# Optimization experiments

Measured on AMD Instinct MI355X. Metric: run time of the kernel, lower is better.

The kernel has to match this reference:

```python
import jax, jax.numpy as jnp
import numpy as np

EPS_NORM = 1e-12  # F.normalize eps
EPS_LOG = 1e-10
COMMITMENT_COST = 0.25


def setup_inputs() -> dict:
    key = jax.random.key(0)
    k1, k2 = jax.random.split(key)
    x = jax.random.normal(k1, (32, 256, 32, 32), dtype=jnp.float32)
    # nn.Embedding weight init: uniform(-1, 1)
    W = jax.random.uniform(k2, (1024, 256), dtype=jnp.float32, minval=-1.0, maxval=1.0)
    return {"x": x, "W": W, "n": 2}


def reference(x, W, n):
    sg = jax.lax.stop_gradient
    # NCHW -> NHWC
    inputs = jnp.transpose(x, (0, 2, 3, 1))
    B, H, Wd, D = inputs.shape
    K = W.shape[0]
    flat = inputs.reshape(-1, D)                       # [N, D]
    N = flat.shape[0]
    # squared euclidean distances via matmul: [N, K]
    distances = (jnp.sum(flat * flat, axis=1, keepdims=True)
                 + jnp.sum(W * W, axis=1)
                 - 2.0 * jnp.matmul(flat, W.T))
    # topk of -distances -> n smallest distances
    neg_vals, encoding_indices = jax.lax.top_k(-distances, n)  # [N, n]
    inv_dist = 1.0 / (-neg_vals)                        # 1/distance, [N, n]
    norm = jnp.maximum(jnp.sqrt(jnp.sum(inv_dist * inv_dist, axis=-1, keepdims=True)), EPS_NORM)
    weights = sg(inv_dist / norm)                       # detached in torch
    # scatter weights into one-hot-ish encodings [N, K]
    rows = jnp.arange(N)[:, None]
    encodings = jnp.zeros((N, K), dtype=flat.dtype).at[rows, encoding_indices].set(weights)
    quantized = jnp.matmul(encodings, W).reshape(B, H, Wd, D)
    e_latent_loss = jnp.mean((sg(quantized) - inputs) ** 2)
    q_latent_loss = jnp.mean((quantized - sg(inputs)) ** 2)
    loss = q_latent_loss + COMMITMENT_COST * e_latent_loss
    # straight-through
    quantized_st = inputs + sg(quantized - inputs)
    avg_probs = jnp.mean(encodings, axis=0)
    perplexity = jnp.exp(-jnp.sum(avg_probs * jnp.log(avg_probs + EPS_LOG)))
    return loss, jnp.transpose(quantized_st, (0, 3, 1, 2)), perplexity, encodings
```

## Files before the change

kernel.cpp:

```cpp
#include <hip/hip_runtime.h>
#include <math.h>

#define NROWS 32768
#define DIMS  256
#define KCODES 1024

typedef __attribute__((ext_vector_type(8))) short short8;
typedef __attribute__((ext_vector_type(4))) float f32x4;

static const size_t OFF_WB     = 8388608;
static const size_t OFF_WNORM  = OFF_WB + 131072;
static const size_t OFF_ENCSUM = OFF_WNORM + 1024;
static const size_t OFF_LOSSP  = OFF_ENCSUM + 1024;
static const size_t OFF_WND    = OFF_LOSSP + 8192;

static const size_t OUT_Q    = 1;
static const size_t OUT_PERP = 8388609;
static const size_t OUT_ENC  = 8388610;

__device__ inline unsigned short f2bf(float f) {
    unsigned int u = __float_as_uint(f);
    unsigned int r = u + 0x7FFFu + ((u >> 16) & 1u);
    return (unsigned short)(r >> 16);
}

__device__ inline float packdi(float d, int code) {
    return __uint_as_float((__float_as_uint(d) & 0xFFFFFC00u) | (unsigned)code);
}

__device__ __forceinline__ void gl_lds16(const void* gsrc, void* ldst) {
    typedef const __attribute__((address_space(1))) unsigned int GU;
    typedef __attribute__((address_space(3))) unsigned int LU;
    __builtin_amdgcn_global_load_lds((GU*)gsrc, (LU*)ldst, 16, 0, 0);
}

__global__ __launch_bounds__(256) void wprep(const float* __restrict__ Wm,
                                             unsigned short* __restrict__ Wb,
                                             float* __restrict__ wnorm,
                                             double* __restrict__ wnormd,
                                             float* __restrict__ enc_sum)
{
    const int r = blockIdx.x * 4 + (threadIdx.x >> 6);
    const int lane = threadIdx.x & 63;
    float4 v = ((const float4*)(Wm + (size_t)r * 256))[lane];
    ushort4 o;
    o.x = f2bf(v.x); o.y = f2bf(v.y); o.z = f2bf(v.z); o.w = f2bf(v.w);
    const int d0 = lane * 4;
    const int kk = d0 >> 5, quad = (d0 >> 3) & 3, jb = d0 & 7;
    const int tt = r >> 4, col = r & 15;
    const size_t idx = (size_t)tt * 4096 + (size_t)((kk * 4 + quad) * 16 + col) * 8 + jb;
    *(ushort4*)(Wb + idx) = o;
    double s = (double)v.x*(double)v.x + (double)v.y*(double)v.y
             + (double)v.z*(double)v.z + (double)v.w*(double)v.w;
    #pragma unroll
    for (int off = 32; off > 0; off >>= 1) s += __shfl_down(s, off);
    if (lane == 0) { wnormd[r] = s; wnorm[r] = (float)s; }
    if (blockIdx.x == 0) {
        #pragma unroll
        for (int q = 0; q < 4; ++q) enc_sum[threadIdx.x * 4 + q] = 0.0f;
    }
}

__global__ __launch_bounds__(512, 4) void gemm_topk_quant(
    const float* __restrict__ x, const unsigned short* __restrict__ Wb,
    const float* __restrict__ wnorm, const double* __restrict__ wnd,
    const float* __restrict__ Wm,
    float* __restrict__ enc_sum,
    float* __restrict__ enc,
    float* __restrict__ outq, float* __restrict__ loss_part)
{
    __shared__ __align__(16) char lds[65536];
    float*  sCd   = (float*)lds;
    float*  qtile = (float*)lds;
    double* rd    = (double*)(lds + 34816);
    double* rnr   = (double*)(lds + 38912);
    int*    s0    = (int*)(lds + 39424);
    int*    s1    = (int*)(lds + 39680);
    float*  sw0   = (float*)(lds + 39936);
    float*  sw1   = (float*)(lds + 40192);
    double* sredd = (double*)(lds + 40448);
    int*    mIdx  = (int*)(lds + 40960);
    unsigned short* xtile = (unsigned short*)(lds + 32768);

    const int t    = threadIdx.x;
    const int wave = t >> 6;
    const int g    = wave & 3;
    const int h    = wave >> 2;
    const int lane = t & 63;
    const int col  = lane & 15;
    const int quad = lane >> 4;
    const int r0   = blockIdx.x * 64;
    const int b    = r0 >> 10;
    const int hw0  = r0 & 1023;
    const float* xblk = x + (size_t)b * 262144 + hw0;

    const int row = t >> 3;
    const int q8  = t & 7;

    const char* wb_bytes = (const char*)Wb;
    const size_t src_wave = (size_t)h * 262144 + (size_t)g * 4096;
    const int    lds_wave = h * 16384 + g * 4096;
    {
        const char* src = wb_bytes + src_wave;
        char* dstl = lds + lds_wave;
        #pragma unroll
        for (int q = 0; q < 4; ++q)
            gl_lds16(src + q * 1024 + lane * 16, dstl + q * 1024);
    }

    float xs[32];
    {
        const float* xr = xblk + row;
        #pragma unroll
        for (int p2 = 0; p2 < 2; ++p2)
            #pragma unroll
            for (int j = 0; j < 16; ++j)
                xs[p2 * 16 + j] = xr[(size_t)(p2 * 128 + q8 * 16 + j) * 1024];
    }

    #pragma unroll
    for (int p2 = 0; p2 < 2; ++p2)
        #pragma unroll
        for (int j4 = 0; j4 < 4; ++j4) {
            ushort4 o;
            o.x = f2bf(xs[p2 * 16 + j4 * 4 + 0]);
            o.y = f2bf(xs[p2 * 16 + j4 * 4 + 1]);
            o.z = f2bf(xs[p2 * 16 + j4 * 4 + 2]);
            o.w = f2bf(xs[p2 * 16 + j4 * 4 + 3]);
            *(ushort4*)(xtile + row * 256 + p2 * 128 + q8 * 16 + j4 * 4) = o;
        }
    __syncthreads();

    short8 af[8];
    #pragma unroll
    for (int kk = 0; kk < 8; ++kk)
        af[kk] = *(const short8*)(xtile + (g * 16 + col) * 256 + kk * 32 + quad * 8);
    __syncthreads();

    float m0[4], m1[4], m2[4];
    #pragma unroll
    for (int r = 0; r < 4; ++r) { m0[r] = 3.4e38f; m1[r] = 3.4e38f; m2[r] = 3.4e38f; }

    for (int cc = 0; cc < 16; ++cc) {
        if (cc < 15) {
            const char* src = wb_bytes + src_wave + (size_t)(cc + 1) * 16384;
            char* dstl = lds + ((cc + 1) & 1) * 32768 + lds_wave;
            #pragma unroll
            for (int q = 0; q < 4; ++q)
                gl_lds16(src + q * 1024 + lane * 16, dstl + q * 1024);
        }
        const char* bb = lds + (cc & 1) * 32768 + h * 16384;
        f32x4 acc0 = {0.f, 0.f, 0.f, 0.f};
        f32x4 acc1 = {0.f, 0.f, 0.f, 0.f};
        #pragma unroll
        for (int kk = 0; kk < 8; ++kk) {
            short8 b0 = *(const short8*)(bb + kk * 1024 + lane * 16);
            short8 b1 = *(const short8*)(bb + 8192 + kk * 1024 + lane * 16);
            acc0 = __builtin_amdgcn_mfma_f32_16x16x32_bf16(af[kk], b0, acc0, 0, 0, 0);
            acc1 = __builtin_amdgcn_mfma_f32_16x16x32_bf16(af[kk], b1, acc1, 0, 0, 0);
        }
        const int code0 = h * 512 + cc * 32 + col;
        const int code1 = code0 + 16;
        const float wn0 = wnorm[code0];
        const float wn1 = wnorm[code1];
        #pragma unroll
        for (int r = 0; r < 4; ++r) {
            float pv0 = packdi(fmaf(-2.0f, acc0[r], wn0), code0);
            float t0  = fmaxf(m0[r], pv0); m0[r] = fminf(m0[r], pv0);
            float t1  = fmaxf(m1[r], t0);  m1[r] = fminf(m1[r], t0);
            m2[r] = fminf(m2[r], t1);
            float pv1 = packdi(fmaf(-2.0f, acc1[r], wn1), code1);
            t0 = fmaxf(m0[r], pv1); m0[r] = fminf(m0[r], pv1);
            t1 = fmaxf(m1[r], t0);  m1[r] = fminf(m1[r], t0);
            m2[r] = fminf(m2[r], t1);
        }
        __syncthreads();
    }

    #pragma unroll
    for (int r = 0; r < 4; ++r) {
        int rl = g * 16 + quad * 4 + r;
        sCd[rl * 96 + h * 48 + col * 3 + 0] = m0[r];
        sCd[rl * 96 + h * 48 + col * 3 + 1] = m1[r];
        sCd[rl * 96 + h * 48 + col * 3 + 2] = m2[r];
    }
    __syncthreads();

    if (t < 64) {
        float bd[8];
        #pragma unroll
        for (int q = 0; q < 8; ++q) bd[q] = 3.4e38f;
        for (int s = 0; s < 96; ++s) {
            float d = sCd[t * 96 + s];
            if (d < bd[7]) {
                bd[7] = d;
                #pragma unroll
                for (int p = 7; p > 0; --p) {
                    if (bd[p] < bd[p-1]) { float tf = bd[p]; bd[p] = bd[p-1]; bd[p-1] = tf; }
                }
            }
        }
        #pragma unroll
        for (int q = 0; q < 8; ++q)
            mIdx[t * 8 + q] = (int)(__float_as_uint(bd[q]) & 1023u);
    }
    __syncthreads();

    {
        int cd[8];
        #pragma unroll
        for (int c8 = 0; c8 < 8; ++c8) cd[c8] = mIdx[row * 8 + c8];
        double dot[8];
        #pragma unroll
        for (int c8 = 0; c8 < 8; ++c8) dot[c8] = 0.0;
        double rn = 0.0;
        #pragma unroll
        for (int v = 0; v < 8; ++v) {
            const int d0 = (v >> 2) * 128 + q8 * 16 + (v & 3) * 4;
            const double x0 = (double)xs[v * 4 + 0];
            const double x1 = (double)xs[v * 4 + 1];
            const double x2 = (double)xs[v * 4 + 2];
            const double x3 = (double)xs[v * 4 + 3];
            rn += x0*x0 + x1*x1 + x2*x2 + x3*x3;
            #pragma unroll
            for (int c8 = 0; c8 < 8; ++c8) {
                const float4 wv = *(const float4*)(Wm + (size_t)cd[c8] * 256 + d0);
                dot[c8] += x0 * (double)wv.x + x1 * (double)wv.y
                         + x2 * (double)wv.z + x3 * (double)wv.w;
            }
        }
        #pragma unroll
        for (int m = 1; m < 8; m <<= 1) {
            #pragma unroll
            for (int c8 = 0; c8 < 8; ++c8) dot[c8] += __shfl_xor(dot[c8], m);
            rn += __shfl_xor(rn, m);
        }
        int myc = 0; double mydot = 0.0;
        #pragma unroll
        for (int c8 = 0; c8 < 8; ++c8)
            if (q8 == c8) { myc = cd[c8]; mydot = dot[c8]; }
        rd[row * 8 + q8] = wnd[myc] - 2.0 * mydot;
        if (q8 == 0) rnr[row] = rn;
    }
    __syncthreads();

    if (t < 64) {
        double rn = rnr[t];
        double d0 = 1e300, d1 = 1e300; int b0 = 1 << 30, b1 = 1 << 30;
        #pragma unroll
        for (int q = 0; q < 8; ++q) {
            double d = rd[t * 8 + q];
            int    c = mIdx[t * 8 + q];
            if (d < d0 || (d == d0 && c < b0)) { d1 = d0; b1 = b0; d0 = d; b0 = c; }
            else if (d < d1 || (d == d1 && c < b1)) { d1 = d; b1 = c; }
        }
        double D0 = rn + d0;
        double D1 = rn + d1;
        double inv0 = 1.0 / D0, inv1 = 1.0 / D1;
        double nrm = sqrt(inv0 * inv0 + inv1 * inv1);
        if (nrm < 1e-12) nrm = 1e-12;
        float w0 = (float)(inv0 / nrm);
        float w1 = (float)(inv1 / nrm);
        s0[t] = b0; s1[t] = b1; sw0[t] = w0; sw1[t] = w1;
        atomicAdd(&enc_sum[b0], w0);
        atomicAdd(&enc_sum[b1], w1);
    }
    __syncthreads();

    #pragma unroll
    for (int rr = 0; rr < 8; ++rr) {
        const int rw = wave * 8 + rr;
        const int i0 = s0[rw], i1 = s1[rw];
        const float w0 = sw0[rw], w1 = sw1[rw];
        f32x4* dst = (f32x4*)(enc + (size_t)(r0 + rw) * KCODES);
        #pragma unroll
        for (int it = 0; it < 4; ++it) {
            const int base = it * 256 + lane * 4;
            f32x4 v;
            v.x = (base + 0 == i0) ? w0 : ((base + 0 == i1) ? w1 : 0.0f);
            v.y = (base + 1 == i0) ? w0 : ((base + 1 == i1) ? w1 : 0.0f);
            v.z = (base + 2 == i0) ? w0 : ((base + 2 == i1) ? w1 : 0.0f);
            v.w = (base + 3 == i0) ? w0 : ((base + 3 == i1) ? w1 : 0.0f);
            __builtin_nontemporal_store(v, &dst[it * 64 + lane]);
        }
    }

    double ls = 0.0;
    #pragma unroll
    for (int p2 = 0; p2 < 2; ++p2) {
        const int   cA = s0[row], cB = s1[row];
        const float w0 = sw0[row], w1 = sw1[row];
        const float* W0 = Wm + (size_t)cA * 256 + p2 * 128 + q8 * 16;
        const float* W1 = Wm + (size_t)cB * 256 + p2 * 128 + q8 * 16;
        #pragma unroll
        for (int v4 = 0; v4 < 4; ++v4) {
            const float4 a  = *(const float4*)(W0 + v4 * 4);
            const float4 bv = *(const float4*)(W1 + v4 * 4);
            float q0 = w0 * a.x + w1 * bv.x;
            float q1 = w0 * a.y + w1 * bv.y;
            float q2 = w0 * a.z + w1 * bv.z;
            float q3 = w0 * a.w + w1 * bv.w;
            float e0 = q0 - xs[p2 * 16 + v4 * 4 + 0];
            float e1 = q1 - xs[p2 * 16 + v4 * 4 + 1];
            float e2 = q2 - xs[p2 * 16 + v4 * 4 + 2];
            float e3 = q3 - xs[p2 * 16 + v4 * 4 + 3];
            ls += (double)(e0*e0 + e1*e1 + e2*e2 + e3*e3);
            const int dl = q8 * 16 + v4 * 4;
            qtile[(dl + 0) * 67 + row] = q0;
            qtile[(dl + 1) * 67 + row] = q1;
            qtile[(dl + 2) * 67 + row] = q2;
            qtile[(dl + 3) * 67 + row] = q3;
        }
        __syncthreads();
        #pragma unroll
        for (int p = 0; p < 4; ++p) {
            const int task = p * 512 + t;
            const int cl   = task >> 4;
            const int hwq  = task & 15;
            f32x4 v;
            v.x = qtile[cl * 67 + hwq * 4 + 0];
            v.y = qtile[cl * 67 + hwq * 4 + 1];
            v.z = qtile[cl * 67 + hwq * 4 + 2];
            v.w = qtile[cl * 67 + hwq * 4 + 3];
            __builtin_nontemporal_store(v,
                (f32x4*)(outq + ((size_t)(b * 256 + p2 * 128 + cl)) * 1024 + hw0 + hwq * 4));
        }
        __syncthreads();
    }

    #pragma unroll
    for (int off = 32; off > 0; off >>= 1) ls += __shfl_down(ls, off);
    if (lane == 0) sredd[wave] = ls;
    __syncthreads();
    if (t == 0) {
        double s = 0.0;
        #pragma unroll
        for (int w = 0; w < 8; ++w) s += sredd[w];
        loss_part[blockIdx.x] = (float)s;
    }
}

__global__ __launch_bounds__(256) void finalize_k(const float* __restrict__ enc_sum,
                                                  const float* __restrict__ loss_part,
                                                  float* __restrict__ out)
{
    __shared__ double sh[256];
    const int t = threadIdx.x;
    double ls = 0.0;
    for (int i = t; i < 512; i += 256) ls += (double)loss_part[i];
    sh[t] = ls; __syncthreads();
    for (int s = 128; s > 0; s >>= 1) { if (t < s) sh[t] += sh[t + s]; __syncthreads(); }
    double loss_sum = sh[0];
    __syncthreads();
    double ps = 0.0;
    for (int k = t; k < KCODES; k += 256) {
        double p = (double)enc_sum[k] / (double)NROWS;
        ps += p * log(p + 1e-10);
    }
    sh[t] = ps; __syncthreads();
    for (int s = 128; s > 0; s >>= 1) { if (t < s) sh[t] += sh[t + s]; __syncthreads(); }
    if (t == 0) {
        out[0]        = (float)(1.25 * loss_sum / 8388608.0);
        out[OUT_PERP] = (float)exp(-sh[0]);
    }
}

extern "C" void kernel_launch(void* const* d_in, const int* in_sizes, int n_in,
                              void* d_out, int out_size, void* d_ws, size_t ws_size,
                              hipStream_t stream)
{
    const float* x  = (const float*)d_in[0];
    const float* Wm = (const float*)d_in[1];
    float* out = (float*)d_out;
    float* ws  = (float*)d_ws;

    unsigned short* Wb      = (unsigned short*)(ws + OFF_WB);
    float*          wnorm   = ws + OFF_WNORM;
    float*          enc_sum = ws + OFF_ENCSUM;
    float*          loss_p  = ws + OFF_LOSSP;
    double*         wnd     = (double*)(ws + OFF_WND);

    wprep<<<KCODES / 4, 256, 0, stream>>>(Wm, Wb, wnorm, wnd, enc_sum);
    gemm_topk_quant<<<NROWS / 64, 512, 0, stream>>>(x, Wb, wnorm, wnd, Wm, enc_sum,
                                                    out + OUT_ENC, out + OUT_Q, loss_p);
    finalize_k<<<1, 256, 0, stream>>>(enc_sum, loss_p, out);
}
```

Before: 272.3 us.

## Swizzle x tile in LDS, parallelize candidate merge across lanes, drop nontemporal stores

The bf16 x tile in LDS is now XOR-swizzled by row so the MFMA fragment reads hit fewer bank conflicts. The top-8 candidate merge, which used to run serially in 64 threads over 96 candidates, is now split across all threads: each of 8 lanes per row keeps a local top-8 of 12 candidates, then the lanes merge with xor shuffles. The candidate buffer is transposed to match. The encodings and quantized outputs now use ordinary stores instead of nontemporal stores, which changes how they interact with the cache.

```diff
diff --git a/kernel.cpp b/kernel.cpp
--- a/kernel.cpp
+++ b/kernel.cpp
@@ -127,14 +127,17 @@
             o.y = f2bf(xs[p2 * 16 + j4 * 4 + 1]);
             o.z = f2bf(xs[p2 * 16 + j4 * 4 + 2]);
             o.w = f2bf(xs[p2 * 16 + j4 * 4 + 3]);
-            *(ushort4*)(xtile + row * 256 + p2 * 128 + q8 * 16 + j4 * 4) = o;
+            const int xi = (row * 256 + p2 * 128 + q8 * 16 + j4 * 4) ^ ((row & 7) << 3);
+            *(ushort4*)(xtile + xi) = o;
         }
     __syncthreads();
 
     short8 af[8];
     #pragma unroll
-    for (int kk = 0; kk < 8; ++kk)
-        af[kk] = *(const short8*)(xtile + (g * 16 + col) * 256 + kk * 32 + quad * 8);
+    for (int kk = 0; kk < 8; ++kk) {
+        const int xi = ((g * 16 + col) * 256 + kk * 32 + quad * 8) ^ ((col & 7) << 3);
+        af[kk] = *(const short8*)(xtile + xi);
+    }
     __syncthreads();
 
     float m0[4], m1[4], m2[4];
@@ -179,30 +182,43 @@
 
     #pragma unroll
     for (int r = 0; r < 4; ++r) {
-        int rl = g * 16 + quad * 4 + r;
-        sCd[rl * 96 + h * 48 + col * 3 + 0] = m0[r];
-        sCd[rl * 96 + h * 48 + col * 3 + 1] = m1[r];
-        sCd[rl * 96 + h * 48 + col * 3 + 2] = m2[r];
-    }
-    __syncthreads();
-
-    if (t < 64) {
-        float bd[8];
-        #pragma unroll
-        for (int q = 0; q < 8; ++q) bd[q] = 3.4e38f;
-        for (int s = 0; s < 96; ++s) {
-            float d = sCd[t * 96 + s];
-            if (d < bd[7]) {
-                bd[7] = d;
-                #pragma unroll
-                for (int p = 7; p > 0; --p) {
-                    if (bd[p] < bd[p-1]) { float tf = bd[p]; bd[p] = bd[p-1]; bd[p-1] = tf; }
-                }
+        const int rl = g * 16 + quad * 4 + r;
+        const int s  = h * 48 + col * 3;
+        sCd[(s + 0) * 66 + rl] = m0[r];
+        sCd[(s + 1) * 66 + rl] = m1[r];
+        sCd[(s + 2) * 66 + rl] = m2[r];
+    }
+    __syncthreads();
+
+    {
+        float a0 = 3.4e38f, a1 = 3.4e38f, a2 = 3.4e38f, a3 = 3.4e38f,
+              a4 = 3.4e38f, a5 = 3.4e38f, a6 = 3.4e38f, a7 = 3.4e38f;
+        #pragma unroll
+        for (int i = 0; i < 12; ++i) {
+            float d = sCd[(q8 * 12 + i) * 66 + row];
+            if (d < a7) {
+                a7 = d; float tf;
+                if (a7 < a6) { tf = a7; a7 = a6; a6 = tf; }
+                if (a6 < a5) { tf = a6; a6 = a5; a5 = tf; }
+                if (a5 < a4) { tf = a5; a5 = a4; a4 = tf; }
+                if (a4 < a3) { tf = a4; a4 = a3; a3 = tf; }
+                if (a3 < a2) { tf = a3; a3 = a2; a2 = tf; }
+                if (a2 < a1) { tf = a2; a2 = a1; a1 = tf; }
+                if (a1 < a0) { tf = a1; a1 = a0; a0 = tf; }
             }
         }
-        #pragma unroll
-        for (int q = 0; q < 8; ++q)
-            mIdx[t * 8 + q] = (int)(__float_as_uint(bd[q]) & 1023u);
+        float sel = 3.4e38f;
+        #pragma unroll
+        for (int q = 0; q < 8; ++q) {
+            float m = a0;
+            m = fminf(m, __shfl_xor(m, 1));
+            m = fminf(m, __shfl_xor(m, 2));
+            m = fminf(m, __shfl_xor(m, 4));
+            if (q8 == q) sel = m;
+            if (a0 == m) { a0 = a1; a1 = a2; a2 = a3; a3 = a4;
+                           a4 = a5; a5 = a6; a6 = a7; a7 = 3.4e38f; }
+        }
+        mIdx[row * 8 + q8] = (int)(__float_as_uint(sel) & 1023u);
     }
     __syncthreads();
 
@@ -281,7 +297,7 @@
             v.y = (base + 1 == i0) ? w0 : ((base + 1 == i1) ? w1 : 0.0f);
             v.z = (base + 2 == i0) ? w0 : ((base + 2 == i1) ? w1 : 0.0f);
             v.w = (base + 3 == i0) ? w0 : ((base + 3 == i1) ? w1 : 0.0f);
-            __builtin_nontemporal_store(v, &dst[it * 64 + lane]);
+            dst[it * 64 + lane] = v;
         }
     }
 
@@ -322,8 +338,7 @@
             v.y = qtile[cl * 67 + hwq * 4 + 1];
             v.z = qtile[cl * 67 + hwq * 4 + 2];
             v.w = qtile[cl * 67 + hwq * 4 + 3];
-            __builtin_nontemporal_store(v,
-                (f32x4*)(outq + ((size_t)(b * 256 + p2 * 128 + cl)) * 1024 + hw0 + hwq * 4));
+            *(f32x4*)(outq + ((size_t)(b * 256 + p2 * 128 + cl)) * 1024 + hw0 + hwq * 4) = v;
         }
         __syncthreads();
     }
```

Result: faster. 263.2 us (-3.3%).
